# Performance work log

Hardware: AMD Instinct MI355X
Metric: run time of the kernel (lower is better)

Reference implementation:

```python
import jax, jax.numpy as jnp
import numpy as np

D_MODEL = 768
NUM_HEADS = 12
D_K = D_MODEL // NUM_HEADS


def setup_inputs() -> dict:
    key = jax.random.key(0)
    ks = jax.random.split(key, 11)
    B, S, D = 2, 4096, D_MODEL
    s = 1.0 / np.sqrt(D)
    return {
        "query": jax.random.normal(ks[0], (B, S, D), jnp.float32),
        "key": jax.random.normal(ks[1], (B, S, D), jnp.float32),
        "value": jax.random.normal(ks[2], (B, S, D), jnp.float32),
        "Wq": jax.random.normal(ks[3], (D, D), jnp.float32) * s,
        "bq": jnp.zeros((D,), jnp.float32),
        "Wk": jax.random.normal(ks[4], (D, D), jnp.float32) * s,
        "bk": jnp.zeros((D,), jnp.float32),
        "Wv": jax.random.normal(ks[5], (D, D), jnp.float32) * s,
        "bv": jnp.zeros((D,), jnp.float32),
        "Wo": jax.random.normal(ks[6], (D, D), jnp.float32) * s,
        "bo": jnp.zeros((D,), jnp.float32),
    }


def reference(query, key, value, Wq, bq, Wk, bk, Wv, bv, Wo, bo):
    B, S, D = query.shape
    H, dk = NUM_HEADS, D_K
    # torch Linear: y = x @ W^T + b
    def proj(x, W, b):
        return (x @ W.T + b).reshape(B, S, H, dk).transpose(0, 2, 1, 3)  # [B,H,S,dk]
    q = proj(query, Wq, bq)
    k = proj(key, Wk, bk)
    v = proj(value, Wv, bv)
    scores = jnp.einsum("bhqd,bhkd->bhqk", q, k) / jnp.sqrt(jnp.float32(dk))
    attn = jax.nn.softmax(scores, axis=-1)  # dropout is identity in eval mode
    x = jnp.einsum("bhqk,bhkd->bhqd", attn, v)
    x = x.transpose(0, 2, 1, 3).reshape(B, S, D)
    return x @ Wo.T + bo
```

## Files before the change

### kernel.cpp

```cpp
#include <hip/hip_runtime.h>
#include <hip/hip_bf16.h>


typedef __attribute__((ext_vector_type(8))) short short8;
typedef __attribute__((ext_vector_type(4))) float floatx4;
typedef __attribute__((ext_vector_type(4))) float float4v;

#define S_LEN 4096
#define D_MODEL 768
#define NUM_HEADS 12
#define DK 64
#define BATCH 2
#define M_ROWS (BATCH * S_LEN)
#define HEADS_TOTAL (BATCH * NUM_HEADS)
#define QSCALE 0.1803368801111204f

__device__ __forceinline__ unsigned short f2bf(float f) {
    union { float f; unsigned int i; } v; v.f = f;
    unsigned int r = v.i + 0x7fff + ((v.i >> 16) & 1);
    return (unsigned short)(r >> 16);
}

__device__ __forceinline__ unsigned int cvt_pk_bf16(float a, float b) {
    unsigned int r;
    asm("v_cvt_pk_bf16_f32 %0, %1, %2" : "=v"(r) : "v"(a), "v"(b));
    return r;
}

__device__ __forceinline__ float exp2_fast(float x) {
    float r;
    asm("v_exp_f32 %0, %1" : "=v"(r) : "v"(x));
    return r;
}

__device__ __forceinline__ int swz(int r, int c) {
    return (r << 6) + ((((c >> 3) ^ (r & 7)) << 3) | (c & 7));
}

__device__ __forceinline__ void pack8(const float4v& f0, const float4v& f1,
                                      unsigned short* __restrict__ dst) {
    uint4 w;
    w.x = cvt_pk_bf16(f0[0], f0[1]);
    w.y = cvt_pk_bf16(f0[2], f0[3]);
    w.z = cvt_pk_bf16(f1[0], f1[1]);
    w.w = cvt_pk_bf16(f1[2], f1[3]);
    *(uint4*)dst = w;
}

template <int MODE, int XF32>
__global__ __launch_bounds__(256, 2) void gemm_bt(
    const void* __restrict__ Xv,
    const float* __restrict__ W,
    const float* __restrict__ bias,
    void* __restrict__ outv,
    int M, int N, int K)
{
    __shared__ __align__(16) unsigned short As[2][8192];
    __shared__ __align__(16) unsigned short Bs[2][8192];

    const int t    = threadIdx.x;
    const int wv   = t >> 6;
    const int lane = t & 63;
    const int l15  = lane & 15;
    const int quad = lane >> 4;
    const int wm   = wv >> 1;
    const int wn   = wv & 1;

    const int bid = blockIdx.y * gridDim.x + blockIdx.x;
    const int wg  = (bid & 7) * 48 + (bid >> 3);
    const int m0  = (wg / 6) * 128;
    const int n0  = (wg % 6) * 128;

    floatx4 acc[4][4];
#pragma unroll
    for (int i = 0; i < 4; ++i)
#pragma unroll
        for (int j = 0; j < 4; ++j) acc[i][j] = (floatx4){0.f, 0.f, 0.f, 0.f};

    const int sr   = t >> 3;
    const int scol = (t & 7) * 8;
    const int st0  = swz(sr, scol);

    float4v xa[8];
    uint4   xu[4];
    float4v wa[8];

#define G_LOAD(step)                                                                     \
    do {                                                                                 \
        const long kofs = (long)(step) * 64;                                             \
        _Pragma("unroll")                                                                \
        for (int p = 0; p < 4; ++p) {                                                    \
            if (XF32) {                                                                  \
                const float* xp = (const float*)Xv + (long)(m0 + sr + 32 * p) * K + kofs + scol; \
                xa[2 * p]     = *(const float4v*)xp;                                     \
                xa[2 * p + 1] = *(const float4v*)(xp + 4);                               \
            } else {                                                                     \
                const unsigned short* xp =                                               \
                    (const unsigned short*)Xv + (long)(m0 + sr + 32 * p) * K + kofs + scol; \
                xu[p] = *(const uint4*)xp;                                               \
            }                                                                            \
            const float* wp = W + (long)(n0 + sr + 32 * p) * K + kofs + scol;            \
            wa[2 * p]     = *(const float4v*)wp;                                         \
            wa[2 * p + 1] = *(const float4v*)(wp + 4);                                   \
        }                                                                                \
    } while (0)

#define G_WRITE(buf)                                                                     \
    do {                                                                                 \
        _Pragma("unroll")                                                                \
        for (int p = 0; p < 4; ++p) {                                                    \
            if (XF32) pack8(xa[2 * p], xa[2 * p + 1], &As[buf][st0 + p * 2048]);         \
            else      *(uint4*)(&As[buf][st0 + p * 2048]) = xu[p];                       \
            pack8(wa[2 * p], wa[2 * p + 1], &Bs[buf][st0 + p * 2048]);                   \
        }                                                                                \
    } while (0)

    const int NS = K / 64;
    G_LOAD(0);
    G_WRITE(0);
    G_LOAD(1);
    __syncthreads();

    int cur = 0;
    for (int s = 0; s < NS; ++s) {
        const unsigned short* Ab = &As[cur][0];
        const unsigned short* Bb = &Bs[cur][0];
#pragma unroll
        for (int kk = 0; kk < 2; ++kk) {
            short8 af[4];
#pragma unroll
            for (int mi = 0; mi < 4; ++mi)
                af[mi] = *(const short8*)(Ab + swz(wm * 64 + mi * 16 + l15, kk * 32 + quad * 8));
#pragma unroll
            for (int nj = 0; nj < 4; ++nj) {
                short8 bf = *(const short8*)(Bb + swz(wn * 64 + nj * 16 + l15, kk * 32 + quad * 8));
#pragma unroll
                for (int mi = 0; mi < 4; ++mi)
                    acc[mi][nj] = __builtin_amdgcn_mfma_f32_16x16x32_bf16(af[mi], bf, acc[mi][nj], 0, 0, 0);
            }
        }
        if (s + 1 < NS) {
            G_WRITE(cur ^ 1);
            if (s + 2 < NS) G_LOAD(s + 2);
            __syncthreads();
            cur ^= 1;
        }
    }
#undef G_LOAD
#undef G_WRITE

    if (MODE == 2) {
        unsigned short* Sx = &As[0][0];
        const int bb2 = m0 >> 12;
        const int h0  = n0 >> 6;
        const int slb = m0 & 4095;
        __syncthreads();
#pragma unroll
        for (int hx = 0; hx < 2; ++hx) {
            if (wn == hx) {
#pragma unroll
                for (int nj = 0; nj < 4; ++nj) {
                    const float bvv = bias[n0 + hx * 64 + nj * 16 + l15];
                    const int col = nj * 16 + l15;
#pragma unroll
                    for (int mi = 0; mi < 4; ++mi)
#pragma unroll
                        for (int reg = 0; reg < 4; ++reg) {
                            const int row = wm * 64 + mi * 16 + quad * 4 + reg;
                            Sx[(row << 6) + (col ^ ((row & 7) << 3))] =
                                f2bf(acc[mi][nj][reg] + bvv);
                        }
                }
            }
            __syncthreads();
#pragma unroll
            for (int p = 0; p < 4; ++p) {
                const int ci = t + (p << 8);
                const int d  = ci >> 4;
                const int s0 = (ci & 15) << 3;
                unsigned short w[8];
#pragma unroll
                for (int j = 0; j < 8; ++j)
                    w[j] = Sx[((s0 + j) << 6) + (d ^ (j << 3))];
                unsigned short* outp = (unsigned short*)outv +
                    ((long)((bb2 * NUM_HEADS + h0 + hx) * DK + d)) * S_LEN + slb + s0;
                *(uint4*)outp = *(uint4*)w;
            }
            __syncthreads();
        }
        return;
    }

#pragma unroll
    for (int nj = 0; nj < 4; ++nj) {
        const int col = n0 + wn * 64 + nj * 16 + l15;
        const float bv = bias[col];
#pragma unroll
        for (int mi = 0; mi < 4; ++mi)
#pragma unroll
            for (int reg = 0; reg < 4; ++reg) {
                const int row = m0 + wm * 64 + mi * 16 + quad * 4 + reg;
                const float o = acc[mi][nj][reg] + bv;
                if (MODE == 0) {
                    ((float*)outv)[(long)row * N + col] = o;
                } else {
                    const int bb = row >> 12;
                    const int ss = row & 4095;
                    const int h  = col >> 6;
                    const int d  = col & 63;
                    ((unsigned short*)outv)[(((long)bb * NUM_HEADS + h) * S_LEN + ss) * DK + d] = f2bf(o);
                }
            }
    }
}

__global__ __launch_bounds__(256, 6) void flash_attn_fused(
    const float* __restrict__ Xq,
    const float* __restrict__ Wq,
    const float* __restrict__ bq,
    const unsigned short* __restrict__ Kg,
    const unsigned short* __restrict__ VTg,
    unsigned short* __restrict__ ctx)
{
    __shared__ __align__(16) unsigned short Ks[4096];
    __shared__ __align__(16) unsigned short Vt[4096];
    __shared__ __align__(16) unsigned short Pq[4096];

    const int t    = threadIdx.x;
    const int wv   = t >> 6;
    const int lane = t & 63;
    const int l15  = lane & 15;
    const int quad = lane >> 4;
    const int q0   = blockIdx.x * 64;
    const int bh   = blockIdx.y;
    const int bb   = bh / NUM_HEADS;
    const int h    = bh % NUM_HEADS;
    const long kbase = (long)bh * S_LEN * DK;
    const long vbase = (long)bh * DK * S_LEN;

    const int srow = t >> 3;
    const int scol = (t & 7) * 8;

    const int st_a = swz(srow, scol);
    const int st_b = swz(32 + srow, scol);

    {
        floatx4 qacc[4];
#pragma unroll
        for (int i = 0; i < 4; ++i) qacc[i] = (floatx4){0.f, 0.f, 0.f, 0.f};

        for (int k0 = 0; k0 < D_MODEL; k0 += 64) {
            {
                const float* xp = Xq + ((long)bb * S_LEN + q0 + srow) * D_MODEL + k0 + scol;
                float4v a0 = *(const float4v*)xp, a1 = *(const float4v*)(xp + 4);
                const float* xp2 = xp + (long)32 * D_MODEL;
                float4v a2 = *(const float4v*)xp2, a3 = *(const float4v*)(xp2 + 4);
                const float* wp = Wq + (long)(h * DK + srow) * D_MODEL + k0 + scol;
                float4v b0 = *(const float4v*)wp, b1 = *(const float4v*)(wp + 4);
                const float* wp2 = wp + (long)32 * D_MODEL;
                float4v b2 = *(const float4v*)wp2, b3 = *(const float4v*)(wp2 + 4);
                pack8(a0, a1, &Ks[st_a]); pack8(a2, a3, &Ks[st_b]);
                pack8(b0, b1, &Vt[st_a]); pack8(b2, b3, &Vt[st_b]);
            }
            __syncthreads();
#pragma unroll
            for (int kk = 0; kk < 2; ++kk) {
                short8 a = *(const short8*)(&Ks[swz(wv * 16 + l15, kk * 32 + quad * 8)]);
#pragma unroll
                for (int nj = 0; nj < 4; ++nj) {
                    short8 b = *(const short8*)(&Vt[swz(nj * 16 + l15, kk * 32 + quad * 8)]);
                    qacc[nj] = __builtin_amdgcn_mfma_f32_16x16x32_bf16(a, b, qacc[nj], 0, 0, 0);
                }
            }
            __syncthreads();
        }
#pragma unroll
        for (int nj = 0; nj < 4; ++nj) {
            const float bv = bq[h * DK + nj * 16 + l15];
#pragma unroll
            for (int reg = 0; reg < 4; ++reg) {
                const int row = wv * 16 + quad * 4 + reg;
                Pq[swz(row, nj * 16 + l15)] = f2bf((qacc[nj][reg] + bv) * QSCALE);
            }
        }
    }

    uint4 kr0 = *(const uint4*)(Kg + kbase + (long)srow * DK + scol);
    uint4 kr1 = *(const uint4*)(Kg + kbase + (long)(32 + srow) * DK + scol);
    uint4 vr0 = *(const uint4*)(VTg + vbase + (long)srow * S_LEN + scol);
    uint4 vr1 = *(const uint4*)(VTg + vbase + (long)(32 + srow) * S_LEN + scol);

    asm volatile("s_waitcnt lgkmcnt(0)" ::: "memory");
    short8 qfrag[2];
#pragma unroll
    for (int kk = 0; kk < 2; ++kk)
        qfrag[kk] = *(const short8*)(&Pq[swz(wv * 16 + l15, kk * 32 + quad * 8)]);

    *(uint4*)(&Ks[st_a]) = kr0; *(uint4*)(&Ks[st_b]) = kr1;
    *(uint4*)(&Vt[st_a]) = vr0; *(uint4*)(&Vt[st_b]) = vr1;
    __syncthreads();

    float l_loc = 0.f;
    floatx4 acc[4];
#pragma unroll
    for (int i = 0; i < 4; ++i) acc[i] = (floatx4){0.f, 0.f, 0.f, 0.f};

    const unsigned short* kp = Kg + kbase + (long)64 * DK;
    const unsigned short* vp = VTg + vbase + 64;

    for (int tix = 0; tix < 64; ++tix) {
        if (tix < 63) {
            kr0 = *(const uint4*)(kp + (long)srow * DK + scol);
            kr1 = *(const uint4*)(kp + (long)(32 + srow) * DK + scol);
            vr0 = *(const uint4*)(vp + (long)srow * S_LEN + scol);
            vr1 = *(const uint4*)(vp + (long)(32 + srow) * S_LEN + scol);
            kp += (long)64 * DK;
            vp += 64;
        }

        floatx4 sc[4];
#pragma unroll
        for (int i = 0; i < 4; ++i) sc[i] = (floatx4){0.f, 0.f, 0.f, 0.f};
        __builtin_amdgcn_s_setprio(1);
#pragma unroll
        for (int kk = 0; kk < 2; ++kk) {
#pragma unroll
            for (int nj = 0; nj < 4; ++nj) {
                short8 kf = *(const short8*)(&Ks[swz(nj * 16 + l15, kk * 32 + quad * 8)]);
                sc[nj] = __builtin_amdgcn_mfma_f32_16x16x32_bf16(kf, qfrag[kk], sc[nj], 0, 0, 0);
            }
        }
        __builtin_amdgcn_s_setprio(0);

#pragma unroll
        for (int nj = 0; nj < 4; ++nj) {
            const float e0 = exp2_fast(sc[nj][0]);
            const float e1 = exp2_fast(sc[nj][1]);
            const float e2 = exp2_fast(sc[nj][2]);
            const float e3 = exp2_fast(sc[nj][3]);
            l_loc += (e0 + e1) + (e2 + e3);
            uint2 w;
            w.x = cvt_pk_bf16(e0, e1);
            w.y = cvt_pk_bf16(e2, e3);
            *(uint2*)(&Pq[swz(wv * 16 + l15, nj * 16 + quad * 4)]) = w;
        }
        asm volatile("s_waitcnt lgkmcnt(0)" ::: "memory");

        __builtin_amdgcn_s_setprio(1);
#pragma unroll
        for (int kk = 0; kk < 2; ++kk) {
            short8 a = *(const short8*)(&Pq[swz(wv * 16 + l15, kk * 32 + quad * 8)]);
#pragma unroll
            for (int dj = 0; dj < 4; ++dj) {
                short8 b = *(const short8*)(&Vt[swz(dj * 16 + l15, kk * 32 + quad * 8)]);
                acc[dj] = __builtin_amdgcn_mfma_f32_16x16x32_bf16(a, b, acc[dj], 0, 0, 0);
            }
        }
        __builtin_amdgcn_s_setprio(0);

        __syncthreads();
        if (tix < 63) {
            *(uint4*)(&Ks[st_a]) = kr0; *(uint4*)(&Ks[st_b]) = kr1;
            *(uint4*)(&Vt[st_a]) = vr0; *(uint4*)(&Vt[st_b]) = vr1;
        }
        __syncthreads();
    }

    float l_full = l_loc;
    l_full += __shfl_xor(l_full, 16);
    l_full += __shfl_xor(l_full, 32);
    float l_row[4];
#pragma unroll
    for (int reg = 0; reg < 4; ++reg)
        l_row[reg] = __shfl(l_full, quad * 4 + reg);
#pragma unroll
    for (int dj = 0; dj < 4; ++dj) {
#pragma unroll
        for (int reg = 0; reg < 4; ++reg) {
            const int ss = q0 + wv * 16 + quad * 4 + reg;
            const float v = acc[dj][reg] / l_row[reg];
            ctx[((long)bb * S_LEN + ss) * D_MODEL + h * DK + dj * 16 + l15] = f2bf(v);
        }
    }
}

__global__ void fill_sentinel(float* out, long n, float val) {
    long i = (long)blockIdx.x * blockDim.x + threadIdx.x;
    if (i < n) out[i] = val;
}

extern "C" void kernel_launch(void* const* d_in, const int* in_sizes, int n_in,
                              void* d_out, int out_size, void* d_ws, size_t ws_size,
                              hipStream_t stream)
{
    const float* q_in = (const float*)d_in[0];
    const float* k_in = (const float*)d_in[1];
    const float* v_in = (const float*)d_in[2];
    const float* Wq = (const float*)d_in[3];
    const float* bq = (const float*)d_in[4];
    const float* Wk = (const float*)d_in[5];
    const float* bk = (const float*)d_in[6];
    const float* Wv = (const float*)d_in[7];
    const float* bv = (const float*)d_in[8];
    const float* Wo = (const float*)d_in[9];
    const float* bo = (const float*)d_in[10];

    const long NELEM = (long)M_ROWS * D_MODEL;
    const size_t needed = (size_t)(3 * NELEM) * sizeof(unsigned short);

    if (ws_size < needed) {
        const long n = (long)out_size;
        fill_sentinel<<<(n + 255) / 256, 256, 0, stream>>>((float*)d_out, n,
                                                           (float)(ws_size >> 20));
        return;
    }

    unsigned short* ws  = (unsigned short*)d_ws;
    unsigned short* kp  = ws;
    unsigned short* vtp = ws + NELEM;
    unsigned short* ctx = ws + 2 * NELEM;

    dim3 ggrid(M_ROWS / 128, D_MODEL / 128);
    gemm_bt<1, 1><<<ggrid, 256, 0, stream>>>(k_in, Wk, bk, kp, M_ROWS, D_MODEL, D_MODEL);
    gemm_bt<2, 1><<<ggrid, 256, 0, stream>>>(v_in, Wv, bv, vtp, M_ROWS, D_MODEL, D_MODEL);

    dim3 agrid(S_LEN / 64, HEADS_TOTAL);
    flash_attn_fused<<<agrid, 256, 0, stream>>>(q_in, Wq, bq, kp, vtp, ctx);

    gemm_bt<0, 0><<<ggrid, 256, 0, stream>>>(ctx, Wo, bo, d_out, M_ROWS, D_MODEL, D_MODEL);
}
```

Before: 402.3 us.

## Retile projection GEMMs to 128x96 with unrolled double-buffer and lighter barriers

Changes the K/V/O projection GEMM tile from 128x128 to 128x96 so the grid grows from 384 to 512 workgroups, which gives a more even wave count across the CUs. The main loop is unrolled by two with separate even and odd register staging sets and fixed LDS buffers. __syncthreads is replaced by an lgkmcnt wait plus s_barrier and a sched_barrier. The V-transpose epilogue now runs in a single pass through a padded (stride 97) LDS tile instead of two passes per head. In exchange, each block gets less reuse per loaded element and uses more registers for the doubled staging buffers.

```diff
diff --git a/kernel.cpp b/kernel.cpp
--- a/kernel.cpp
+++ b/kernel.cpp
@@ -45,6 +45,12 @@
     w.z = cvt_pk_bf16(f1[0], f1[1]);
     w.w = cvt_pk_bf16(f1[2], f1[3]);
     *(uint4*)dst = w;
+}
+
+__device__ __forceinline__ void bar_lgkm() {
+    asm volatile("s_waitcnt lgkmcnt(0)" ::: "memory");
+    __builtin_amdgcn_s_barrier();
+    __builtin_amdgcn_sched_barrier(0);
 }
 
 template <int MODE, int XF32>
@@ -56,7 +62,7 @@
     int M, int N, int K)
 {
     __shared__ __align__(16) unsigned short As[2][8192];
-    __shared__ __align__(16) unsigned short Bs[2][8192];
+    __shared__ __align__(16) unsigned short Bs[2][6144];
 
     const int t    = threadIdx.x;
     const int wv   = t >> 6;
@@ -66,134 +72,145 @@
     const int wm   = wv >> 1;
     const int wn   = wv & 1;
 
-    const int bid = blockIdx.y * gridDim.x + blockIdx.x;
-    const int wg  = (bid & 7) * 48 + (bid >> 3);
-    const int m0  = (wg / 6) * 128;
-    const int n0  = (wg % 6) * 128;
-
-    floatx4 acc[4][4];
+    const int bid = blockIdx.x;
+    const int wg  = (bid & 7) * 64 + (bid >> 3);
+    const int m0  = (wg >> 3) * 128;
+    const int n0  = (wg & 7) * 96;
+
+    floatx4 acc[4][3];
 #pragma unroll
     for (int i = 0; i < 4; ++i)
 #pragma unroll
-        for (int j = 0; j < 4; ++j) acc[i][j] = (floatx4){0.f, 0.f, 0.f, 0.f};
+        for (int j = 0; j < 3; ++j) acc[i][j] = (floatx4){0.f, 0.f, 0.f, 0.f};
 
     const int sr   = t >> 3;
     const int scol = (t & 7) * 8;
     const int st0  = swz(sr, scol);
 
-    float4v xa[8];
-    uint4   xu[4];
-    float4v wa[8];
-
-#define G_LOAD(step)                                                                     \
+    float4v xaE[8], xaO[8];
+    uint4   xuE[4], xuO[4];
+    float4v waE[6], waO[6];
+
+#define G_LOAD(xa, xu, wa, step)                                                         \
     do {                                                                                 \
-        const long kofs = (long)(step) * 64;                                             \
+        const long kofs = (long)(step) * 64 + scol;                                      \
         _Pragma("unroll")                                                                \
         for (int p = 0; p < 4; ++p) {                                                    \
             if (XF32) {                                                                  \
-                const float* xp = (const float*)Xv + (long)(m0 + sr + 32 * p) * K + kofs + scol; \
+                const float* xp = (const float*)Xv + (long)(m0 + sr + 32 * p) * K + kofs; \
                 xa[2 * p]     = *(const float4v*)xp;                                     \
                 xa[2 * p + 1] = *(const float4v*)(xp + 4);                               \
             } else {                                                                     \
                 const unsigned short* xp =                                               \
-                    (const unsigned short*)Xv + (long)(m0 + sr + 32 * p) * K + kofs + scol; \
+                    (const unsigned short*)Xv + (long)(m0 + sr + 32 * p) * K + kofs;     \
                 xu[p] = *(const uint4*)xp;                                               \
             }                                                                            \
-            const float* wp = W + (long)(n0 + sr + 32 * p) * K + kofs + scol;            \
+        }                                                                                \
+        _Pragma("unroll")                                                                \
+        for (int p = 0; p < 3; ++p) {                                                    \
+            const float* wp = W + (long)(n0 + sr + 32 * p) * K + kofs;                   \
             wa[2 * p]     = *(const float4v*)wp;                                         \
             wa[2 * p + 1] = *(const float4v*)(wp + 4);                                   \
         }                                                                                \
     } while (0)
 
-#define G_WRITE(buf)                                                                     \
+#define G_WRITE(xa, xu, wa, buf)                                                         \
     do {                                                                                 \
         _Pragma("unroll")                                                                \
         for (int p = 0; p < 4; ++p) {                                                    \
             if (XF32) pack8(xa[2 * p], xa[2 * p + 1], &As[buf][st0 + p * 2048]);         \
             else      *(uint4*)(&As[buf][st0 + p * 2048]) = xu[p];                       \
+        }                                                                                \
+        _Pragma("unroll")                                                                \
+        for (int p = 0; p < 3; ++p)                                                      \
             pack8(wa[2 * p], wa[2 * p + 1], &Bs[buf][st0 + p * 2048]);                   \
+    } while (0)
+
+#define DO_MFMA(buf)                                                                     \
+    do {                                                                                 \
+        const unsigned short* Ab = &As[buf][0];                                          \
+        const unsigned short* Bb = &Bs[buf][0];                                          \
+        _Pragma("unroll")                                                                \
+        for (int kk = 0; kk < 2; ++kk) {                                                 \
+            short8 af[4];                                                                \
+            _Pragma("unroll")                                                            \
+            for (int mi = 0; mi < 4; ++mi)                                               \
+                af[mi] = *(const short8*)(Ab + swz(wm * 64 + mi * 16 + l15, kk * 32 + quad * 8)); \
+            _Pragma("unroll")                                                            \
+            for (int nj = 0; nj < 3; ++nj) {                                             \
+                short8 bf = *(const short8*)(Bb + swz(wn * 48 + nj * 16 + l15, kk * 32 + quad * 8)); \
+                _Pragma("unroll")                                                        \
+                for (int mi = 0; mi < 4; ++mi)                                           \
+                    acc[mi][nj] = __builtin_amdgcn_mfma_f32_16x16x32_bf16(af[mi], bf, acc[mi][nj], 0, 0, 0); \
+            }                                                                            \
         }                                                                                \
     } while (0)
 
     const int NS = K / 64;
-    G_LOAD(0);
-    G_WRITE(0);
-    G_LOAD(1);
+
+    G_LOAD(xaE, xuE, waE, 0);
+    G_WRITE(xaE, xuE, waE, 0);
+    G_LOAD(xaO, xuO, waO, 1);
     __syncthreads();
 
-    int cur = 0;
-    for (int s = 0; s < NS; ++s) {
-        const unsigned short* Ab = &As[cur][0];
-        const unsigned short* Bb = &Bs[cur][0];
-#pragma unroll
-        for (int kk = 0; kk < 2; ++kk) {
-            short8 af[4];
-#pragma unroll
-            for (int mi = 0; mi < 4; ++mi)
-                af[mi] = *(const short8*)(Ab + swz(wm * 64 + mi * 16 + l15, kk * 32 + quad * 8));
-#pragma unroll
-            for (int nj = 0; nj < 4; ++nj) {
-                short8 bf = *(const short8*)(Bb + swz(wn * 64 + nj * 16 + l15, kk * 32 + quad * 8));
-#pragma unroll
-                for (int mi = 0; mi < 4; ++mi)
-                    acc[mi][nj] = __builtin_amdgcn_mfma_f32_16x16x32_bf16(af[mi], bf, acc[mi][nj], 0, 0, 0);
-            }
-        }
-        if (s + 1 < NS) {
-            G_WRITE(cur ^ 1);
-            if (s + 2 < NS) G_LOAD(s + 2);
-            __syncthreads();
-            cur ^= 1;
-        }
-    }
+    for (int s = 0; s < NS - 2; s += 2) {
+        DO_MFMA(0);
+        G_WRITE(xaO, xuO, waO, 1);
+        G_LOAD(xaE, xuE, waE, s + 2);
+        bar_lgkm();
+        DO_MFMA(1);
+        G_WRITE(xaE, xuE, waE, 0);
+        if (s + 3 < NS) G_LOAD(xaO, xuO, waO, s + 3);
+        bar_lgkm();
+    }
+    DO_MFMA(0);
+    G_WRITE(xaO, xuO, waO, 1);
+    bar_lgkm();
+    DO_MFMA(1);
+
 #undef G_LOAD
 #undef G_WRITE
+#undef DO_MFMA
 
     if (MODE == 2) {
         unsigned short* Sx = &As[0][0];
+        __syncthreads();
+#pragma unroll
+        for (int nj = 0; nj < 3; ++nj) {
+            const int colL = wn * 48 + nj * 16 + l15;
+            const float bvv = bias[n0 + colL];
+#pragma unroll
+            for (int mi = 0; mi < 4; ++mi)
+#pragma unroll
+                for (int reg = 0; reg < 4; ++reg) {
+                    const int row = wm * 64 + mi * 16 + quad * 4 + reg;
+                    Sx[row * 97 + colL] = f2bf(acc[mi][nj][reg] + bvv);
+                }
+        }
+        __syncthreads();
         const int bb2 = m0 >> 12;
-        const int h0  = n0 >> 6;
         const int slb = m0 & 4095;
-        __syncthreads();
-#pragma unroll
-        for (int hx = 0; hx < 2; ++hx) {
-            if (wn == hx) {
-#pragma unroll
-                for (int nj = 0; nj < 4; ++nj) {
-                    const float bvv = bias[n0 + hx * 64 + nj * 16 + l15];
-                    const int col = nj * 16 + l15;
-#pragma unroll
-                    for (int mi = 0; mi < 4; ++mi)
-#pragma unroll
-                        for (int reg = 0; reg < 4; ++reg) {
-                            const int row = wm * 64 + mi * 16 + quad * 4 + reg;
-                            Sx[(row << 6) + (col ^ ((row & 7) << 3))] =
-                                f2bf(acc[mi][nj][reg] + bvv);
-                        }
-                }
-            }
-            __syncthreads();
-#pragma unroll
-            for (int p = 0; p < 4; ++p) {
-                const int ci = t + (p << 8);
-                const int d  = ci >> 4;
-                const int s0 = (ci & 15) << 3;
-                unsigned short w[8];
-#pragma unroll
-                for (int j = 0; j < 8; ++j)
-                    w[j] = Sx[((s0 + j) << 6) + (d ^ (j << 3))];
-                unsigned short* outp = (unsigned short*)outv +
-                    ((long)((bb2 * NUM_HEADS + h0 + hx) * DK + d)) * S_LEN + slb + s0;
-                *(uint4*)outp = *(uint4*)w;
-            }
-            __syncthreads();
+#pragma unroll
+        for (int p = 0; p < 6; ++p) {
+            const int ci   = t + (p << 8);
+            const int colL = ci >> 4;
+            const int s8   = (ci & 15) << 3;
+            const int dg   = n0 + colL;
+            const int h    = dg >> 6;
+            const int d    = dg & 63;
+            unsigned short w[8];
+#pragma unroll
+            for (int j = 0; j < 8; ++j) w[j] = Sx[(s8 + j) * 97 + colL];
+            unsigned short* outp = (unsigned short*)outv +
+                ((long)((bb2 * NUM_HEADS + h) * DK + d)) * S_LEN + slb + s8;
+            *(uint4*)outp = *(uint4*)w;
         }
         return;
     }
 
 #pragma unroll
-    for (int nj = 0; nj < 4; ++nj) {
-        const int col = n0 + wn * 64 + nj * 16 + l15;
+    for (int nj = 0; nj < 3; ++nj) {
+        const int col = n0 + wn * 48 + nj * 16 + l15;
         const float bv = bias[col];
 #pragma unroll
         for (int mi = 0; mi < 4; ++mi)
@@ -420,12 +437,12 @@
     unsigned short* vtp = ws + NELEM;
     unsigned short* ctx = ws + 2 * NELEM;
 
-    dim3 ggrid(M_ROWS / 128, D_MODEL / 128);
-    gemm_bt<1, 1><<<ggrid, 256, 0, stream>>>(k_in, Wk, bk, kp, M_ROWS, D_MODEL, D_MODEL);
-    gemm_bt<2, 1><<<ggrid, 256, 0, stream>>>(v_in, Wv, bv, vtp, M_ROWS, D_MODEL, D_MODEL);
+    const int GG = (M_ROWS / 128) * (D_MODEL / 96);
+    gemm_bt<1, 1><<<GG, 256, 0, stream>>>(k_in, Wk, bk, kp, M_ROWS, D_MODEL, D_MODEL);
+    gemm_bt<2, 1><<<GG, 256, 0, stream>>>(v_in, Wv, bv, vtp, M_ROWS, D_MODEL, D_MODEL);
 
     dim3 agrid(S_LEN / 64, HEADS_TOTAL);
     flash_attn_fused<<<agrid, 256, 0, stream>>>(q_in, Wq, bq, kp, vtp, ctx);
 
-    gemm_bt<0, 0><<<ggrid, 256, 0, stream>>>(ctx, Wo, bo, d_out, M_ROWS, D_MODEL, D_MODEL);
-}
+    gemm_bt<0, 0><<<GG, 256, 0, stream>>>(ctx, Wo, bo, d_out, M_ROWS, D_MODEL, D_MODEL);
+}
```

New measurement: 381.2 us. 5.3% less time.
